# Kernel tuning notes

Measured on AMD Instinct MI355X. Metric: run time of the kernel, lower is better.

The kernel has to match this reference:

```python
import jax, jax.numpy as jnp
import numpy as np

N = 100000   # nodes
E = 1600000  # edges
NEG_SLOPE = 0.2
EPS = 1e-16


def _layer_norm(x, g, b):
    mu = jnp.mean(x, axis=-1, keepdims=True)
    var = jnp.mean((x - mu) ** 2, axis=-1, keepdims=True)
    return (x - mu) * jax.lax.rsqrt(var + 1e-5) * g + b


def _gat_layer(x, W, att_s, att_d, bias, src, dst, heads, C):
    n = x.shape[0]
    h = (x @ W.T).reshape(n, heads, C)            # [N,H,C]
    sa = jnp.sum(h * att_s, axis=-1)              # [N,H]
    da = jnp.sum(h * att_d, axis=-1)              # [N,H]
    logits = jax.nn.leaky_relu(sa[src] + da[dst], NEG_SLOPE)  # [E,H]
    m = jax.ops.segment_max(logits, dst, num_segments=n)      # [N,H]
    m = jnp.where(jnp.isfinite(m), m, 0.0)
    w = jnp.exp(logits - m[dst])                  # [E,H]
    denom = jax.ops.segment_sum(w, dst, num_segments=n)       # [N,H]
    msg = h[src] * w[:, :, None]                  # [E,H,C]
    agg = jax.ops.segment_sum(msg, dst, num_segments=n)       # [N,H,C]
    agg = agg / jnp.maximum(denom, EPS)[:, :, None]
    out = (agg + h).reshape(n, heads * C) + bias  # residual + bias
    return out


def setup_inputs() -> dict:
    key = jax.random.key(0)
    ks = jax.random.split(key, 16)
    s = 0.05
    inp = {
        "x": jax.random.normal(ks[0], (N, 128), jnp.float32),
        "edge_src": jax.random.randint(ks[1], (E,), 0, N, jnp.int32),
        "edge_dst": jax.random.randint(ks[2], (E,), 0, N, jnp.int32),
        # layer 1: in 128 -> heads=2, C=32 (out width 64)
        "W1": jax.random.normal(ks[3], (64, 128), jnp.float32) * s,
        "as1": jax.random.normal(ks[4], (2, 32), jnp.float32) * s,
        "ad1": jax.random.normal(ks[5], (2, 32), jnp.float32) * s,
        "b1": jnp.zeros((64,), jnp.float32),
        # layer 2: 64 -> heads=2, C=32
        "W2": jax.random.normal(ks[6], (64, 64), jnp.float32) * s,
        "as2": jax.random.normal(ks[7], (2, 32), jnp.float32) * s,
        "ad2": jax.random.normal(ks[8], (2, 32), jnp.float32) * s,
        "b2": jnp.zeros((64,), jnp.float32),
        # layer 3 (last): 64 -> heads=1, C=32
        "W3": jax.random.normal(ks[9], (32, 64), jnp.float32) * s,
        "as3": jax.random.normal(ks[10], (1, 32), jnp.float32) * s,
        "ad3": jax.random.normal(ks[11], (1, 32), jnp.float32) * s,
        "b3": jnp.zeros((32,), jnp.float32),
        "gamma1": jnp.ones((64,), jnp.float32),
        "beta1": jnp.zeros((64,), jnp.float32),
        "gamma2": jnp.ones((64,), jnp.float32),
        "beta2": jnp.zeros((64,), jnp.float32),
    }
    return inp


def reference(x, edge_src, edge_dst, W1, as1, ad1, b1, W2, as2, ad2, b2,
              W3, as3, ad3, b3, gamma1, beta1, gamma2, beta2):
    h = _gat_layer(x, W1, as1, ad1, b1, edge_src, edge_dst, 2, 32)
    h = jax.nn.relu(_layer_norm(h, gamma1, beta1))
    h = _gat_layer(h, W2, as2, ad2, b2, edge_src, edge_dst, 2, 32)
    h = jax.nn.relu(_layer_norm(h, gamma2, beta2))
    h = _gat_layer(h, W3, as3, ad3, b3, edge_src, edge_dst, 1, 32)
    return h
```

## Files before the change

kernel.cpp:

```cpp
#include <hip/hip_runtime.h>
#include <hip/hip_fp16.h>

#define LEAKY 0.2f
#define BSH 7
#define BN 128
#define CHUNK 4096
#define NBMAX 1024

__device__ __forceinline__ float leaky(float l) {
  return l >= 0.f ? l : LEAKY * l;
}

typedef _Float16 f16x2 __attribute__((ext_vector_type(2)));

__device__ __forceinline__ float fdot2(unsigned a, unsigned b, float c) {
#if __has_builtin(__builtin_amdgcn_fdot2)
  return __builtin_amdgcn_fdot2(__builtin_bit_cast(f16x2, a),
                                __builtin_bit_cast(f16x2, b), c, false);
#else
  __half2 ha = *(__half2*)&a, hb = *(__half2*)&b;
  float2 fa = __half22float2(ha), fb = __half22float2(hb);
  return fmaf(fa.x, fb.x, fmaf(fa.y, fb.y, c));
#endif
}

__device__ __forceinline__ int packsplat(float w) {
  const __half2 s = __half2half2(__float2half(w));
  return *(const int*)&s;
}
__device__ __forceinline__ __half2 asH2(unsigned u) { return *(__half2*)&u; }

template<int K, int CO, int H, bool IN_F32>
__global__ __launch_bounds__(256, 6)
void gat_gemm3(const void* __restrict__ xin, const float* __restrict__ W,
               const float* __restrict__ atts, const float* __restrict__ attd,
               __half* __restrict__ hh, float* __restrict__ sa, float* __restrict__ da,
               int N) {
  constexpr int CG = CO / 4;
  constexpr int BM = (256 / CG) * 4;
  constexpr int BK = 64;
  constexpr int NK = K / BK;
  constexpr int C = CO / H;
  constexpr int LDW = BK / 2 + 4;

  __shared__ unsigned xs[BM][LDW];
  __shared__ unsigned ws[CO][LDW];

  const int t = (int)threadIdx.x;
  const int cg = t % CG;
  const int ng = t / CG;
  const int n0 = (int)blockIdx.x * BM;

  float acc[4][4] = {};

  for (int kb = 0; kb < NK; ++kb) {
    __syncthreads();
    if constexpr (IN_F32) {
      const float* x = (const float*)xin;
      constexpr int F4R = BK / 4;
      constexpr int TOT = BM * F4R;
      for (int f = t; f < TOT; f += 256) {
        const int r = f / F4R, c = f % F4R;
        int row = n0 + r; row = row < N ? row : N - 1;
        const float4 v = *(const float4*)(x + (size_t)row * K + kb * BK + c * 4);
        const __half2 h0 = __floats2half2_rn(v.x, v.y);
        const __half2 h1 = __floats2half2_rn(v.z, v.w);
        xs[r][c * 2]     = *(const unsigned*)&h0;
        xs[r][c * 2 + 1] = *(const unsigned*)&h1;
      }
    } else {
      const __half* x = (const __half*)xin;
      constexpr int U4R = BK / 8;
      constexpr int TOT = BM * U4R;
      for (int f = t; f < TOT; f += 256) {
        const int r = f / U4R, c = f % U4R;
        int row = n0 + r; row = row < N ? row : N - 1;
        const uint4 v = *(const uint4*)(x + (size_t)row * K + kb * BK + c * 8);
        *(uint4*)&xs[r][c * 4] = v;
      }
    }
    {
      constexpr int F4R = BK / 4;
      constexpr int TOT = CO * F4R;
      for (int f = t; f < TOT; f += 256) {
        const int r = f / F4R, c = f % F4R;
        const float4 v = *(const float4*)(W + (size_t)r * K + kb * BK + c * 4);
        const __half2 h0 = __floats2half2_rn(v.x, v.y);
        const __half2 h1 = __floats2half2_rn(v.z, v.w);
        ws[r][c * 2]     = *(const unsigned*)&h0;
        ws[r][c * 2 + 1] = *(const unsigned*)&h1;
      }
    }
    __syncthreads();
    #pragma unroll
    for (int k = 0; k < BK; k += 8) {
      uint4 xa[4], wb[4];
      #pragma unroll
      for (int i = 0; i < 4; ++i) xa[i] = *(const uint4*)&xs[ng * 4 + i][k / 2];
      #pragma unroll
      for (int j = 0; j < 4; ++j) wb[j] = *(const uint4*)&ws[cg + CG * j][k / 2];
      #pragma unroll
      for (int i = 0; i < 4; ++i) {
        #pragma unroll
        for (int j = 0; j < 4; ++j) {
          acc[i][j] = fdot2(xa[i].x, wb[j].x, acc[i][j]);
          acc[i][j] = fdot2(xa[i].y, wb[j].y, acc[i][j]);
          acc[i][j] = fdot2(xa[i].z, wb[j].z, acc[i][j]);
          acc[i][j] = fdot2(xa[i].w, wb[j].w, acc[i][j]);
        }
      }
    }
  }

  float as_[4], ad_[4];
  #pragma unroll
  for (int j = 0; j < 4; ++j) {
    as_[j] = atts[cg + CG * j];
    ad_[j] = attd[cg + CG * j];
  }
  float ps[4][H] = {}, pd[4][H] = {};
  #pragma unroll
  for (int i = 0; i < 4; ++i) {
    #pragma unroll
    for (int j = 0; j < 4; ++j) {
      const int hd = (CG * j) / C;
      ps[i][hd] = fmaf(acc[i][j], as_[j], ps[i][hd]);
      pd[i][hd] = fmaf(acc[i][j], ad_[j], pd[i][hd]);
    }
  }
  #pragma unroll
  for (int m = 1; m < CG; m <<= 1) {
    #pragma unroll
    for (int i = 0; i < 4; ++i) {
      #pragma unroll
      for (int hd = 0; hd < H; ++hd) {
        ps[i][hd] += __shfl_xor(ps[i][hd], m, 64);
        pd[i][hd] += __shfl_xor(pd[i][hd], m, 64);
      }
    }
  }

  #pragma unroll
  for (int i = 0; i < 4; ++i) {
    const int n = n0 + ng * 4 + i;
    if (n < N) {
      #pragma unroll
      for (int j = 0; j < 4; ++j)
        hh[(size_t)n * CO + cg + CG * j] = __float2half(acc[i][j]);
      if (cg == 0) {
        #pragma unroll
        for (int hd = 0; hd < H; ++hd) {
          sa[n * H + hd] = ps[i][hd];
          da[n * H + hd] = pd[i][hd];
        }
      }
    }
  }
}

__global__ __launch_bounds__(256)
void gat_edge2(const __half* __restrict__ hh,
               const float* __restrict__ sa, const float* __restrict__ da,
               const int* __restrict__ rowp, const int* __restrict__ col,
               const float* __restrict__ bias, const float* __restrict__ gamma,
               const float* __restrict__ beta, __half* __restrict__ out, int N) {
  __shared__ int2 wst[4][4][17][2];
  const int t = (int)threadIdx.x;
  const int lane = t & 63;
  const int wib = t >> 6;
  const int quarter = lane >> 4;
  const int l = lane & 15;
  const int headq = l >> 3;
  const int wgl = (int)((blockIdx.x * blockDim.x + t) >> 6);
  const int n = wgl * 4 + quarter;
  const bool valid = (n < N);
  const int nc = valid ? n : N - 1;
  const int beg = rowp[nc];
  const int end = rowp[nc + 1];
  const float2 dvv = *(const float2*)(da + (size_t)nc * 2);
  const __half2* __restrict__ hhp = (const __half2*)hh;

  const __half2 z = __float2half2_rn(0.f);
  __half2 aL0 = z, aH0 = z, aL1 = z, aH1 = z, aL2 = z, aH2 = z, aL3 = z, aH3 = z;
  __half2 q0 = z, q1 = z;

  int sP = 0; float2 pP = make_float2(0.f, 0.f);
  if (beg < end) {
    const int cnt0 = min(16, end - beg);
    if (l < cnt0) {
      sP = col[beg + l];
      pP = *(const float2*)(sa + (size_t)sP * 2);
    }
  }

  for (int b0 = beg; b0 < end; b0 += 16) {
    const int cnt = min(16, end - b0);
    if (l < cnt) {
      int2 e0; e0.x = sP; e0.y = packsplat(__expf(leaky(pP.x + dvv.x)));
      int2 e1; e1.x = sP; e1.y = packsplat(__expf(leaky(pP.y + dvv.y)));
      wst[wib][quarter][l][0] = e0;
      wst[wib][quarter][l][1] = e1;
    }
    const int nb0 = b0 + 16;
    if (nb0 < end) {
      const int ncnt = min(16, end - nb0);
      if (l < ncnt) {
        sP = col[nb0 + l];
        pP = *(const float2*)(sa + (size_t)sP * 2);
      }
    }
    int i = 0;
    for (; i + 8 <= cnt; i += 8) {
      int2 e[8];
      #pragma unroll
      for (int j = 0; j < 8; ++j) e[j] = wst[wib][quarter][i + j][headq];
      uint2 hv[8];
      #pragma unroll
      for (int j = 0; j < 8; ++j) hv[j] = *(const uint2*)(hhp + ((size_t)e[j].x << 5) + 2 * l);
      __half2 w[8];
      #pragma unroll
      for (int j = 0; j < 8; ++j) w[j] = asH2(e[j].y);
      q0 = __hadd2(q0, __hadd2(__hadd2(w[0], w[1]), __hadd2(w[2], w[3])));
      q1 = __hadd2(q1, __hadd2(__hadd2(w[4], w[5]), __hadd2(w[6], w[7])));
      aL0 = __hfma2(w[0], asH2(hv[0].x), aL0); aH0 = __hfma2(w[0], asH2(hv[0].y), aH0);
      aL1 = __hfma2(w[1], asH2(hv[1].x), aL1); aH1 = __hfma2(w[1], asH2(hv[1].y), aH1);
      aL2 = __hfma2(w[2], asH2(hv[2].x), aL2); aH2 = __hfma2(w[2], asH2(hv[2].y), aH2);
      aL3 = __hfma2(w[3], asH2(hv[3].x), aL3); aH3 = __hfma2(w[3], asH2(hv[3].y), aH3);
      aL0 = __hfma2(w[4], asH2(hv[4].x), aL0); aH0 = __hfma2(w[4], asH2(hv[4].y), aH0);
      aL1 = __hfma2(w[5], asH2(hv[5].x), aL1); aH1 = __hfma2(w[5], asH2(hv[5].y), aH1);
      aL2 = __hfma2(w[6], asH2(hv[6].x), aL2); aH2 = __hfma2(w[6], asH2(hv[6].y), aH2);
      aL3 = __hfma2(w[7], asH2(hv[7].x), aL3); aH3 = __hfma2(w[7], asH2(hv[7].y), aH3);
    }
    for (; i + 4 <= cnt; i += 4) {
      int2 e[4];
      #pragma unroll
      for (int j = 0; j < 4; ++j) e[j] = wst[wib][quarter][i + j][headq];
      uint2 hv[4];
      #pragma unroll
      for (int j = 0; j < 4; ++j) hv[j] = *(const uint2*)(hhp + ((size_t)e[j].x << 5) + 2 * l);
      __half2 w[4];
      #pragma unroll
      for (int j = 0; j < 4; ++j) w[j] = asH2(e[j].y);
      q0 = __hadd2(q0, __hadd2(__hadd2(w[0], w[1]), __hadd2(w[2], w[3])));
      aL0 = __hfma2(w[0], asH2(hv[0].x), aL0); aH0 = __hfma2(w[0], asH2(hv[0].y), aH0);
      aL1 = __hfma2(w[1], asH2(hv[1].x), aL1); aH1 = __hfma2(w[1], asH2(hv[1].y), aH1);
      aL2 = __hfma2(w[2], asH2(hv[2].x), aL2); aH2 = __hfma2(w[2], asH2(hv[2].y), aH2);
      aL3 = __hfma2(w[3], asH2(hv[3].x), aL3); aH3 = __hfma2(w[3], asH2(hv[3].y), aH3);
    }
    for (; i < cnt; ++i) {
      const int2 e = wst[wib][quarter][i][headq];
      const uint2 hv = *(const uint2*)(hhp + ((size_t)e.x << 5) + 2 * l);
      const __half2 w = asH2(e.y);
      q0 = __hadd2(q0, w);
      aL0 = __hfma2(w, asH2(hv.x), aL0);
      aH0 = __hfma2(w, asH2(hv.y), aH0);
    }
  }

  const float c0 = (__low2float(aL0) + __low2float(aL1)) + (__low2float(aL2) + __low2float(aL3));
  const float c1 = (__high2float(aL0) + __high2float(aL1)) + (__high2float(aL2) + __high2float(aL3));
  const float c2 = (__low2float(aH0) + __low2float(aH1)) + (__low2float(aH2) + __low2float(aH3));
  const float c3 = (__high2float(aH0) + __high2float(aH1)) + (__high2float(aH2) + __high2float(aH3));
  const float qf = __low2float(q0) + __low2float(q1);

  const float inv = 1.f / fmaxf(qf, 1e-16f);
  const uint2 hr = *(const uint2*)(hhp + ((size_t)nc << 5) + 2 * l);
  const float2 r01 = __half22float2(asH2(hr.x));
  const float2 r23 = __half22float2(asH2(hr.y));
  const float4 bi = *(const float4*)(bias + 4 * l);
  float v0 = c0 * inv + r01.x + bi.x;
  float v1 = c1 * inv + r01.y + bi.y;
  float v2 = c2 * inv + r23.x + bi.z;
  float v3 = c3 * inv + r23.y + bi.w;
  {
    float s = (v0 + v1) + (v2 + v3);
    #pragma unroll
    for (int m = 1; m < 16; m <<= 1) s += __shfl_xor(s, m, 64);
    const float mu = s * (1.f / 64.f);
    const float d0 = v0 - mu, d1 = v1 - mu, d2 = v2 - mu, d3 = v3 - mu;
    float vs = (d0 * d0 + d1 * d1) + (d2 * d2 + d3 * d3);
    #pragma unroll
    for (int m = 1; m < 16; m <<= 1) vs += __shfl_xor(vs, m, 64);
    const float rs = rsqrtf(vs * (1.f / 64.f) + 1e-5f);
    const float4 g = *(const float4*)(gamma + 4 * l);
    const float4 be = *(const float4*)(beta + 4 * l);
    v0 = fmaxf(d0 * rs * g.x + be.x, 0.f);
    v1 = fmaxf(d1 * rs * g.y + be.y, 0.f);
    v2 = fmaxf(d2 * rs * g.z + be.z, 0.f);
    v3 = fmaxf(d3 * rs * g.w + be.w, 0.f);
  }
  if (valid) {
    const __half2 o01 = __floats2half2_rn(v0, v1);
    const __half2 o23 = __floats2half2_rn(v2, v3);
    uint2 o; o.x = *(const unsigned*)&o01; o.y = *(const unsigned*)&o23;
    *(uint2*)(out + (size_t)n * 64 + 4 * l) = o;
  }
}

__global__ __launch_bounds__(256)
void gat_edge1(const __half* __restrict__ hh,
               const float* __restrict__ sa, const float* __restrict__ da,
               const int* __restrict__ rowp, const int* __restrict__ col,
               const float* __restrict__ bias, float* __restrict__ out, int N) {
  __shared__ int2 wst[4][8][9];
  const int t = (int)threadIdx.x;
  const int lane = t & 63;
  const int wib = t >> 6;
  const int oct = lane >> 3;
  const int l = lane & 7;
  const int wgl = (int)((blockIdx.x * blockDim.x + t) >> 6);
  const int n = wgl * 8 + oct;
  const bool valid = (n < N);
  const int nc = valid ? n : N - 1;
  const int beg = rowp[nc];
  const int end = rowp[nc + 1];
  const float dv = da[nc];
  const __half2* __restrict__ hhp = (const __half2*)hh;

  const __half2 z = __float2half2_rn(0.f);
  __half2 aL0 = z, aH0 = z, aL1 = z, aH1 = z, aL2 = z, aH2 = z, aL3 = z, aH3 = z;
  __half2 q0 = z, q1 = z;

  int sP = 0; float pP = 0.f;
  if (beg < end) {
    const int cnt0 = min(8, end - beg);
    if (l < cnt0) { sP = col[beg + l]; pP = sa[sP]; }
  }

  for (int b0 = beg; b0 < end; b0 += 8) {
    const int cnt = min(8, end - b0);
    if (l < cnt) {
      int2 e; e.x = sP; e.y = packsplat(__expf(leaky(pP + dv)));
      wst[wib][oct][l] = e;
    }
    const int nb0 = b0 + 8;
    if (nb0 < end) {
      const int ncnt = min(8, end - nb0);
      if (l < ncnt) { sP = col[nb0 + l]; pP = sa[sP]; }
    }
    int i = 0;
    for (; i + 8 <= cnt; i += 8) {
      int2 e[8];
      #pragma unroll
      for (int j = 0; j < 8; ++j) e[j] = wst[wib][oct][i + j];
      uint2 hv[8];
      #pragma unroll
      for (int j = 0; j < 8; ++j) hv[j] = *(const uint2*)(hhp + ((size_t)e[j].x << 4) + 2 * l);
      __half2 w[8];
      #pragma unroll
      for (int j = 0; j < 8; ++j) w[j] = asH2(e[j].y);
      q0 = __hadd2(q0, __hadd2(__hadd2(w[0], w[1]), __hadd2(w[2], w[3])));
      q1 = __hadd2(q1, __hadd2(__hadd2(w[4], w[5]), __hadd2(w[6], w[7])));
      aL0 = __hfma2(w[0], asH2(hv[0].x), aL0); aH0 = __hfma2(w[0], asH2(hv[0].y), aH0);
      aL1 = __hfma2(w[1], asH2(hv[1].x), aL1); aH1 = __hfma2(w[1], asH2(hv[1].y), aH1);
      aL2 = __hfma2(w[2], asH2(hv[2].x), aL2); aH2 = __hfma2(w[2], asH2(hv[2].y), aH2);
      aL3 = __hfma2(w[3], asH2(hv[3].x), aL3); aH3 = __hfma2(w[3], asH2(hv[3].y), aH3);
      aL0 = __hfma2(w[4], asH2(hv[4].x), aL0); aH0 = __hfma2(w[4], asH2(hv[4].y), aH0);
      aL1 = __hfma2(w[5], asH2(hv[5].x), aL1); aH1 = __hfma2(w[5], asH2(hv[5].y), aH1);
      aL2 = __hfma2(w[6], asH2(hv[6].x), aL2); aH2 = __hfma2(w[6], asH2(hv[6].y), aH2);
      aL3 = __hfma2(w[7], asH2(hv[7].x), aL3); aH3 = __hfma2(w[7], asH2(hv[7].y), aH3);
    }
    for (; i + 4 <= cnt; i += 4) {
      int2 e[4];
      #pragma unroll
      for (int j = 0; j < 4; ++j) e[j] = wst[wib][oct][i + j];
      uint2 hv[4];
      #pragma unroll
      for (int j = 0; j < 4; ++j) hv[j] = *(const uint2*)(hhp + ((size_t)e[j].x << 4) + 2 * l);
      __half2 w[4];
      #pragma unroll
      for (int j = 0; j < 4; ++j) w[j] = asH2(e[j].y);
      q0 = __hadd2(q0, __hadd2(__hadd2(w[0], w[1]), __hadd2(w[2], w[3])));
      aL0 = __hfma2(w[0], asH2(hv[0].x), aL0); aH0 = __hfma2(w[0], asH2(hv[0].y), aH0);
      aL1 = __hfma2(w[1], asH2(hv[1].x), aL1); aH1 = __hfma2(w[1], asH2(hv[1].y), aH1);
      aL2 = __hfma2(w[2], asH2(hv[2].x), aL2); aH2 = __hfma2(w[2], asH2(hv[2].y), aH2);
      aL3 = __hfma2(w[3], asH2(hv[3].x), aL3); aH3 = __hfma2(w[3], asH2(hv[3].y), aH3);
    }
    for (; i < cnt; ++i) {
      const int2 e = wst[wib][oct][i];
      const uint2 hv = *(const uint2*)(hhp + ((size_t)e.x << 4) + 2 * l);
      const __half2 w = asH2(e.y);
      q0 = __hadd2(q0, w);
      aL0 = __hfma2(w, asH2(hv.x), aL0);
      aH0 = __hfma2(w, asH2(hv.y), aH0);
    }
  }

  const float c0 = (__low2float(aL0) + __low2float(aL1)) + (__low2float(aL2) + __low2float(aL3));
  const float c1 = (__high2float(aL0) + __high2float(aL1)) + (__high2float(aL2) + __high2float(aL3));
  const float c2 = (__low2float(aH0) + __low2float(aH1)) + (__low2float(aH2) + __low2float(aH3));
  const float c3 = (__high2float(aH0) + __high2float(aH1)) + (__high2float(aH2) + __high2float(aH3));
  const float qf = __low2float(q0) + __low2float(q1);

  if (valid) {
    const float inv = 1.f / fmaxf(qf, 1e-16f);
    const uint2 hr = *(const uint2*)(hhp + ((size_t)nc << 4) + 2 * l);
    const float2 r01 = __half22float2(asH2(hr.x));
    const float2 r23 = __half22float2(asH2(hr.y));
    const float4 bi = *(const float4*)(bias + 4 * l);
    float4 o;
    o.x = c0 * inv + r01.x + bi.x;
    o.y = c1 * inv + r01.y + bi.y;
    o.z = c2 * inv + r23.x + bi.z;
    o.w = c3 * inv + r23.y + bi.w;
    *(float4*)(out + (size_t)n * 32 + 4 * l) = o;
  }
}


__global__ __launch_bounds__(256)
void k_hist_chunk(const int* __restrict__ dst, int* __restrict__ cntmat,
                  int E, int NB, int NW) {
  __shared__ int lh[NBMAX];
  const int t = (int)threadIdx.x;
  const int chunk = (int)blockIdx.x;
  const int c0 = chunk * CHUNK;
  const int cnt = min(CHUNK, E - c0);
  for (int b = t; b < NB; b += 256) lh[b] = 0;
  __syncthreads();
  for (int i = t; i < cnt; i += 256)
    atomicAdd(&lh[dst[c0 + i] >> BSH], 1);
  __syncthreads();
  for (int b = t; b < NB; b += 256)
    cntmat[(size_t)b * NW + chunk] = lh[b];
}

template<int VPT>
__global__ __launch_bounds__(256)
void k_colscan(int* __restrict__ cntmat, int* __restrict__ bcnt, int NW) {
  __shared__ int sm[256];
  const int b = (int)blockIdx.x;
  int* row = cntmat + (size_t)b * NW;
  const int t = (int)threadIdx.x;
  int v[VPT];
  int run = 0;
  #pragma unroll
  for (int j = 0; j < VPT; ++j) {
    const int c = t * VPT + j;
    v[j] = (c < NW) ? row[c] : 0;
    run += v[j];
  }
  sm[t] = run;
  __syncthreads();
  #pragma unroll
  for (int off = 1; off < 256; off <<= 1) {
    int xv = (t >= off) ? sm[t - off] : 0;
    __syncthreads();
    sm[t] += xv;
    __syncthreads();
  }
  int excl = sm[t] - run;
  #pragma unroll
  for (int j = 0; j < VPT; ++j) {
    const int c = t * VPT + j;
    if (c < NW) row[c] = excl;
    excl += v[j];
  }
  if (t == 255) bcnt[b] = sm[255];
}

__global__ void k_bscan(const int* __restrict__ bcnt, int nb,
                        int* __restrict__ bstart, int* __restrict__ rowp_last, int E) {
  __shared__ int sm[256];
  const int t = (int)threadIdx.x;
  int v[4];
  #pragma unroll
  for (int j = 0; j < 4; ++j) { int i = t * 4 + j; v[j] = (i < nb) ? bcnt[i] : 0; }
  const int tot = v[0] + v[1] + v[2] + v[3];
  sm[t] = tot; __syncthreads();
  #pragma unroll
  for (int off = 1; off < 256; off <<= 1) {
    int xv = (t >= off) ? sm[t - off] : 0;
    __syncthreads();
    sm[t] += xv;
    __syncthreads();
  }
  int excl = sm[t] - tot;
  #pragma unroll
  for (int j = 0; j < 4; ++j) {
    int i = t * 4 + j;
    if (i < nb) { bstart[i] = excl; excl += v[j]; }
  }
  if (t == 0) { bstart[nb] = E; *rowp_last = E; }
}

__global__ __launch_bounds__(256)
void k_part(const int* __restrict__ src, const int* __restrict__ dst,
            const int* __restrict__ bstart, const int* __restrict__ cntmat,
            int* __restrict__ pairs, int E, int NB, int NW) {
  __shared__ int lh[NBMAX];
  __shared__ int lofs[NBMAX];
  __shared__ int gofs[NBMAX];
  __shared__ int stg[CHUNK];
  __shared__ short stgb[CHUNK];
  __shared__ int bsum[256];
  const int t = (int)threadIdx.x;
  const int chunk = (int)blockIdx.x;
  const int c0 = chunk * CHUNK;
  const int cnt = min(CHUNK, E - c0);

  for (int b = t; b < NB; b += 256) lh[b] = 0;
  __syncthreads();
  for (int i = t; i < cnt; i += 256)
    atomicAdd(&lh[dst[c0 + i] >> BSH], 1);
  __syncthreads();

  int v[4]; int run = 0;
  #pragma unroll
  for (int j = 0; j < 4; ++j) {
    const int b = t * 4 + j;
    v[j] = (b < NB) ? lh[b] : 0;
    run += v[j];
  }
  bsum[t] = run;
  __syncthreads();
  #pragma unroll
  for (int off = 1; off < 256; off <<= 1) {
    int xv = (t >= off) ? bsum[t - off] : 0;
    __syncthreads();
    bsum[t] += xv;
    __syncthreads();
  }
  int base = bsum[t] - run;
  #pragma unroll
  for (int j = 0; j < 4; ++j) {
    const int b = t * 4 + j;
    if (b < NB) lofs[b] = base;
    base += v[j];
  }
  __syncthreads();

  for (int b = t; b < NB; b += 256) {
    gofs[b] = bstart[b] + cntmat[(size_t)b * NW + chunk];
    lh[b] = lofs[b];
  }
  __syncthreads();

  for (int i = t; i < cnt; i += 256) {
    const int d = dst[c0 + i];
    const int b = d >> BSH;
    const int p = atomicAdd(&lh[b], 1);
    stg[p] = (src[c0 + i] << BSH) | (d & (BN - 1));
    stgb[p] = (short)b;
  }
  __syncthreads();

  for (int i = t; i < cnt; i += 256) {
    const int b = (int)stgb[i];
    pairs[gofs[b] + (i - lofs[b])] = stg[i];
  }
}

__global__ __launch_bounds__(256)
void k_bucket_csr(const int* __restrict__ pairs, const int* __restrict__ bstart,
                  int* __restrict__ rowp, int* __restrict__ col, int N) {
  __shared__ int ldeg[BN];
  __shared__ int lofs[BN];
  const int b = (int)blockIdx.x;
  const int t = (int)threadIdx.x;
  const int base = b << BSH;
  const int nn = min(BN, N - base);
  const int s0 = bstart[b];
  const int s1 = bstart[b + 1];

  if (t < BN) ldeg[t] = 0;
  __syncthreads();
  for (int i = s0 + t; i < s1; i += 256)
    atomicAdd(&ldeg[pairs[i] & (BN - 1)], 1);
  __syncthreads();
  if (t < BN) lofs[t] = ldeg[t];
  __syncthreads();
  #pragma unroll
  for (int off = 1; off < BN; off <<= 1) {
    int v = (t < BN && t >= off) ? lofs[t - off] : 0;
    __syncthreads();
    if (t < BN) lofs[t] += v;
    __syncthreads();
  }
  if (t < BN) {
    const int ofs = s0 + lofs[t] - ldeg[t];
    if (t < nn) rowp[base + t] = ofs;
    ldeg[t] = ofs;
  }
  __syncthreads();
  for (int i = s0 + t; i < s1; i += 256) {
    const int pr = pairs[i];
    const int p = atomicAdd(&ldeg[pr & (BN - 1)], 1);
    col[p] = pr >> BSH;
  }
}

extern "C" void kernel_launch(void* const* d_in, const int* in_sizes, int n_in,
                              void* d_out, int out_size, void* d_ws, size_t ws_size,
                              hipStream_t stream) {
  const float* x   = (const float*)d_in[0];
  const int* esrc  = (const int*)d_in[1];
  const int* edst  = (const int*)d_in[2];
  const float* W1  = (const float*)d_in[3];
  const float* as1 = (const float*)d_in[4];
  const float* ad1 = (const float*)d_in[5];
  const float* b1  = (const float*)d_in[6];
  const float* W2  = (const float*)d_in[7];
  const float* as2 = (const float*)d_in[8];
  const float* ad2 = (const float*)d_in[9];
  const float* b2  = (const float*)d_in[10];
  const float* W3  = (const float*)d_in[11];
  const float* as3 = (const float*)d_in[12];
  const float* ad3 = (const float*)d_in[13];
  const float* b3  = (const float*)d_in[14];
  const float* g1  = (const float*)d_in[15];
  const float* be1 = (const float*)d_in[16];
  const float* g2  = (const float*)d_in[17];
  const float* be2 = (const float*)d_in[18];

  const int N = in_sizes[0] / 128;
  const int E = in_sizes[1];
  const int NB = (N + BN - 1) / BN;
  const int NW = (E + CHUNK - 1) / CHUNK;

  char* ws = (char*)d_ws;
  size_t off = 0;
  auto alloc = [&](size_t bytes) -> void* {
    void* p = ws + off;
    off = (off + bytes + 255) & ~(size_t)255;
    return p;
  };
  __half* lnbuf = (__half*)alloc((size_t)N * 64 * 2);
  __half* hh   = (__half*)alloc((size_t)N * 64 * 2);
  float* sab   = (float*)alloc((size_t)N * 2 * 4);
  float* dab   = (float*)alloc((size_t)N * 2 * 4);
  int* rowp    = (int*)alloc((size_t)(N + 1) * 4);
  int* colb    = (int*)alloc((size_t)E * 4);
  int* bcnt    = (int*)alloc((size_t)NB * 4);
  int* bstart  = (int*)alloc((size_t)(NB + 1) * 4);
  int* cntmat  = (int*)alloc((size_t)NB * NW * 4);
  int* pairs = (E <= out_size) ? (int*)d_out : (int*)alloc((size_t)E * 4);
  (void)ws_size; (void)n_in;

  k_hist_chunk<<<NW, 256, 0, stream>>>(edst, cntmat, E, NB, NW);
  if (NW <= 512)        k_colscan<2><<<NB, 256, 0, stream>>>(cntmat, bcnt, NW);
  else if (NW <= 1024)  k_colscan<4><<<NB, 256, 0, stream>>>(cntmat, bcnt, NW);
  else                  k_colscan<8><<<NB, 256, 0, stream>>>(cntmat, bcnt, NW);
  k_bscan<<<1, 256, 0, stream>>>(bcnt, NB, bstart, rowp + N, E);
  k_part<<<NW, 256, 0, stream>>>(esrc, edst, bstart, cntmat, pairs, E, NB, NW);
  k_bucket_csr<<<NB, 256, 0, stream>>>(pairs, bstart, rowp, colb, N);

  const int gG12 = (N + 63) / 64;
  const int gG3  = (N + 127) / 128;
  const int gE2 = (N + 15) / 16;
  const int gE1 = (N + 31) / 32;

  gat_gemm3<128, 64, 2, true><<<gG12, 256, 0, stream>>>(x, W1, as1, ad1, hh, sab, dab, N);
  gat_edge2<<<gE2, 256, 0, stream>>>(hh, sab, dab, rowp, colb, b1, g1, be1, lnbuf, N);

  gat_gemm3<64, 64, 2, false><<<gG12, 256, 0, stream>>>(lnbuf, W2, as2, ad2, hh, sab, dab, N);
  gat_edge2<<<gE2, 256, 0, stream>>>(hh, sab, dab, rowp, colb, b2, g2, be2, lnbuf, N);

  gat_gemm3<64, 32, 1, false><<<gG3, 256, 0, stream>>>(lnbuf, W3, as3, ad3, hh, sab, dab, N);
  gat_edge1<<<gE1, 256, 0, stream>>>(hh, sab, dab, rowp, colb, b3, (float*)d_out, N);
}
```

Baseline: 220.2 us.

## Halve lanes per node in GAT edge kernels using 16-byte feature gathers

The edge aggregation kernels now assign fewer lanes per destination node: 8 lanes per node for the two-head layers (previously 16) and 4 lanes per node for the final layer (previously 8). Each lane gathers 8 halves per neighbour with uint4 loads instead of 4 halves with uint2 loads, and the grids shrink to match. The aim is fewer, wider memory requests per edge and more nodes per wavefront, which should cut per-edge loop overhead and divergence from uneven degrees. In exchange each lane has less unrolling (4 edges per batch instead of 8) and holds more accumulators, and the batch sizes for edge-weight staging shrink.

```diff
diff --git a/kernel.cpp b/kernel.cpp
--- a/kernel.cpp
+++ b/kernel.cpp
@@ -164,249 +164,244 @@
                const int* __restrict__ rowp, const int* __restrict__ col,
                const float* __restrict__ bias, const float* __restrict__ gamma,
                const float* __restrict__ beta, __half* __restrict__ out, int N) {
-  __shared__ int2 wst[4][4][17][2];
-  const int t = (int)threadIdx.x;
-  const int lane = t & 63;
-  const int wib = t >> 6;
-  const int quarter = lane >> 4;
-  const int l = lane & 15;
-  const int headq = l >> 3;
-  const int wgl = (int)((blockIdx.x * blockDim.x + t) >> 6);
-  const int n = wgl * 4 + quarter;
-  const bool valid = (n < N);
-  const int nc = valid ? n : N - 1;
-  const int beg = rowp[nc];
-  const int end = rowp[nc + 1];
-  const float2 dvv = *(const float2*)(da + (size_t)nc * 2);
-  const __half2* __restrict__ hhp = (const __half2*)hh;
-
-  const __half2 z = __float2half2_rn(0.f);
-  __half2 aL0 = z, aH0 = z, aL1 = z, aH1 = z, aL2 = z, aH2 = z, aL3 = z, aH3 = z;
-  __half2 q0 = z, q1 = z;
-
-  int sP = 0; float2 pP = make_float2(0.f, 0.f);
-  if (beg < end) {
-    const int cnt0 = min(16, end - beg);
-    if (l < cnt0) {
-      sP = col[beg + l];
-      pP = *(const float2*)(sa + (size_t)sP * 2);
-    }
-  }
-
-  for (int b0 = beg; b0 < end; b0 += 16) {
-    const int cnt = min(16, end - b0);
-    if (l < cnt) {
-      int2 e0; e0.x = sP; e0.y = packsplat(__expf(leaky(pP.x + dvv.x)));
-      int2 e1; e1.x = sP; e1.y = packsplat(__expf(leaky(pP.y + dvv.y)));
-      wst[wib][quarter][l][0] = e0;
-      wst[wib][quarter][l][1] = e1;
-    }
-    const int nb0 = b0 + 16;
-    if (nb0 < end) {
-      const int ncnt = min(16, end - nb0);
-      if (l < ncnt) {
-        sP = col[nb0 + l];
-        pP = *(const float2*)(sa + (size_t)sP * 2);
-      }
-    }
-    int i = 0;
-    for (; i + 8 <= cnt; i += 8) {
-      int2 e[8];
-      #pragma unroll
-      for (int j = 0; j < 8; ++j) e[j] = wst[wib][quarter][i + j][headq];
-      uint2 hv[8];
-      #pragma unroll
-      for (int j = 0; j < 8; ++j) hv[j] = *(const uint2*)(hhp + ((size_t)e[j].x << 5) + 2 * l);
-      __half2 w[8];
-      #pragma unroll
-      for (int j = 0; j < 8; ++j) w[j] = asH2(e[j].y);
-      q0 = __hadd2(q0, __hadd2(__hadd2(w[0], w[1]), __hadd2(w[2], w[3])));
-      q1 = __hadd2(q1, __hadd2(__hadd2(w[4], w[5]), __hadd2(w[6], w[7])));
-      aL0 = __hfma2(w[0], asH2(hv[0].x), aL0); aH0 = __hfma2(w[0], asH2(hv[0].y), aH0);
-      aL1 = __hfma2(w[1], asH2(hv[1].x), aL1); aH1 = __hfma2(w[1], asH2(hv[1].y), aH1);
-      aL2 = __hfma2(w[2], asH2(hv[2].x), aL2); aH2 = __hfma2(w[2], asH2(hv[2].y), aH2);
-      aL3 = __hfma2(w[3], asH2(hv[3].x), aL3); aH3 = __hfma2(w[3], asH2(hv[3].y), aH3);
-      aL0 = __hfma2(w[4], asH2(hv[4].x), aL0); aH0 = __hfma2(w[4], asH2(hv[4].y), aH0);
-      aL1 = __hfma2(w[5], asH2(hv[5].x), aL1); aH1 = __hfma2(w[5], asH2(hv[5].y), aH1);
-      aL2 = __hfma2(w[6], asH2(hv[6].x), aL2); aH2 = __hfma2(w[6], asH2(hv[6].y), aH2);
-      aL3 = __hfma2(w[7], asH2(hv[7].x), aL3); aH3 = __hfma2(w[7], asH2(hv[7].y), aH3);
-    }
-    for (; i + 4 <= cnt; i += 4) {
-      int2 e[4];
-      #pragma unroll
-      for (int j = 0; j < 4; ++j) e[j] = wst[wib][quarter][i + j][headq];
-      uint2 hv[4];
-      #pragma unroll
-      for (int j = 0; j < 4; ++j) hv[j] = *(const uint2*)(hhp + ((size_t)e[j].x << 5) + 2 * l);
-      __half2 w[4];
-      #pragma unroll
-      for (int j = 0; j < 4; ++j) w[j] = asH2(e[j].y);
-      q0 = __hadd2(q0, __hadd2(__hadd2(w[0], w[1]), __hadd2(w[2], w[3])));
-      aL0 = __hfma2(w[0], asH2(hv[0].x), aL0); aH0 = __hfma2(w[0], asH2(hv[0].y), aH0);
-      aL1 = __hfma2(w[1], asH2(hv[1].x), aL1); aH1 = __hfma2(w[1], asH2(hv[1].y), aH1);
-      aL2 = __hfma2(w[2], asH2(hv[2].x), aL2); aH2 = __hfma2(w[2], asH2(hv[2].y), aH2);
-      aL3 = __hfma2(w[3], asH2(hv[3].x), aL3); aH3 = __hfma2(w[3], asH2(hv[3].y), aH3);
-    }
-    for (; i < cnt; ++i) {
-      const int2 e = wst[wib][quarter][i][headq];
-      const uint2 hv = *(const uint2*)(hhp + ((size_t)e.x << 5) + 2 * l);
-      const __half2 w = asH2(e.y);
-      q0 = __hadd2(q0, w);
-      aL0 = __hfma2(w, asH2(hv.x), aL0);
-      aH0 = __hfma2(w, asH2(hv.y), aH0);
-    }
-  }
-
-  const float c0 = (__low2float(aL0) + __low2float(aL1)) + (__low2float(aL2) + __low2float(aL3));
-  const float c1 = (__high2float(aL0) + __high2float(aL1)) + (__high2float(aL2) + __high2float(aL3));
-  const float c2 = (__low2float(aH0) + __low2float(aH1)) + (__low2float(aH2) + __low2float(aH3));
-  const float c3 = (__high2float(aH0) + __high2float(aH1)) + (__high2float(aH2) + __high2float(aH3));
-  const float qf = __low2float(q0) + __low2float(q1);
-
-  const float inv = 1.f / fmaxf(qf, 1e-16f);
-  const uint2 hr = *(const uint2*)(hhp + ((size_t)nc << 5) + 2 * l);
-  const float2 r01 = __half22float2(asH2(hr.x));
-  const float2 r23 = __half22float2(asH2(hr.y));
-  const float4 bi = *(const float4*)(bias + 4 * l);
-  float v0 = c0 * inv + r01.x + bi.x;
-  float v1 = c1 * inv + r01.y + bi.y;
-  float v2 = c2 * inv + r23.x + bi.z;
-  float v3 = c3 * inv + r23.y + bi.w;
-  {
-    float s = (v0 + v1) + (v2 + v3);
-    #pragma unroll
-    for (int m = 1; m < 16; m <<= 1) s += __shfl_xor(s, m, 64);
-    const float mu = s * (1.f / 64.f);
-    const float d0 = v0 - mu, d1 = v1 - mu, d2 = v2 - mu, d3 = v3 - mu;
-    float vs = (d0 * d0 + d1 * d1) + (d2 * d2 + d3 * d3);
-    #pragma unroll
-    for (int m = 1; m < 16; m <<= 1) vs += __shfl_xor(vs, m, 64);
-    const float rs = rsqrtf(vs * (1.f / 64.f) + 1e-5f);
-    const float4 g = *(const float4*)(gamma + 4 * l);
-    const float4 be = *(const float4*)(beta + 4 * l);
-    v0 = fmaxf(d0 * rs * g.x + be.x, 0.f);
-    v1 = fmaxf(d1 * rs * g.y + be.y, 0.f);
-    v2 = fmaxf(d2 * rs * g.z + be.z, 0.f);
-    v3 = fmaxf(d3 * rs * g.w + be.w, 0.f);
-  }
-  if (valid) {
-    const __half2 o01 = __floats2half2_rn(v0, v1);
-    const __half2 o23 = __floats2half2_rn(v2, v3);
-    uint2 o; o.x = *(const unsigned*)&o01; o.y = *(const unsigned*)&o23;
-    *(uint2*)(out + (size_t)n * 64 + 4 * l) = o;
-  }
-}
-
-__global__ __launch_bounds__(256)
-void gat_edge1(const __half* __restrict__ hh,
-               const float* __restrict__ sa, const float* __restrict__ da,
-               const int* __restrict__ rowp, const int* __restrict__ col,
-               const float* __restrict__ bias, float* __restrict__ out, int N) {
-  __shared__ int2 wst[4][8][9];
+  __shared__ int2 wst[4][8][9][2];
   const int t = (int)threadIdx.x;
   const int lane = t & 63;
   const int wib = t >> 6;
   const int oct = lane >> 3;
   const int l = lane & 7;
+  const int headq = l >> 2;
   const int wgl = (int)((blockIdx.x * blockDim.x + t) >> 6);
   const int n = wgl * 8 + oct;
   const bool valid = (n < N);
   const int nc = valid ? n : N - 1;
   const int beg = rowp[nc];
   const int end = rowp[nc + 1];
-  const float dv = da[nc];
-  const __half2* __restrict__ hhp = (const __half2*)hh;
+  const float2 dvv = *(const float2*)(da + (size_t)nc * 2);
+  const __half* __restrict__ hp = hh;
 
   const __half2 z = __float2half2_rn(0.f);
-  __half2 aL0 = z, aH0 = z, aL1 = z, aH1 = z, aL2 = z, aH2 = z, aL3 = z, aH3 = z;
-  __half2 q0 = z, q1 = z;
-
-  int sP = 0; float pP = 0.f;
+  __half2 A0 = z, A1 = z, A2 = z, A3 = z;
+  __half2 B0 = z, B1 = z, B2 = z, B3 = z;
+  __half2 qA = z, qB = z;
+
+  int sP = 0; float2 pP = make_float2(0.f, 0.f);
   if (beg < end) {
-    const int cnt0 = min(8, end - beg);
-    if (l < cnt0) { sP = col[beg + l]; pP = sa[sP]; }
+    const int c0 = min(8, end - beg);
+    if (l < c0) { sP = col[beg + l]; pP = *(const float2*)(sa + (size_t)sP * 2); }
   }
 
   for (int b0 = beg; b0 < end; b0 += 8) {
     const int cnt = min(8, end - b0);
     if (l < cnt) {
-      int2 e; e.x = sP; e.y = packsplat(__expf(leaky(pP + dv)));
-      wst[wib][oct][l] = e;
+      int2 e0; e0.x = sP; e0.y = packsplat(__expf(leaky(pP.x + dvv.x)));
+      int2 e1; e1.x = sP; e1.y = packsplat(__expf(leaky(pP.y + dvv.y)));
+      wst[wib][oct][l][0] = e0;
+      wst[wib][oct][l][1] = e1;
     }
     const int nb0 = b0 + 8;
     if (nb0 < end) {
       const int ncnt = min(8, end - nb0);
+      if (l < ncnt) { sP = col[nb0 + l]; pP = *(const float2*)(sa + (size_t)sP * 2); }
+    }
+    int i = 0;
+    for (; i + 4 <= cnt; i += 4) {
+      const int2 e0 = wst[wib][oct][i][headq];
+      const int2 e1 = wst[wib][oct][i + 1][headq];
+      const int2 e2 = wst[wib][oct][i + 2][headq];
+      const int2 e3 = wst[wib][oct][i + 3][headq];
+      const uint4 h0 = *(const uint4*)(hp + ((size_t)e0.x << 6) + 8 * l);
+      const uint4 h1 = *(const uint4*)(hp + ((size_t)e1.x << 6) + 8 * l);
+      const uint4 h2 = *(const uint4*)(hp + ((size_t)e2.x << 6) + 8 * l);
+      const uint4 h3 = *(const uint4*)(hp + ((size_t)e3.x << 6) + 8 * l);
+      const __half2 w0 = asH2(e0.y), w1 = asH2(e1.y), w2 = asH2(e2.y), w3 = asH2(e3.y);
+      qA = __hadd2(qA, __hadd2(w0, w1));
+      qB = __hadd2(qB, __hadd2(w2, w3));
+      A0 = __hfma2(w0, asH2(h0.x), A0); A1 = __hfma2(w0, asH2(h0.y), A1);
+      A2 = __hfma2(w0, asH2(h0.z), A2); A3 = __hfma2(w0, asH2(h0.w), A3);
+      B0 = __hfma2(w1, asH2(h1.x), B0); B1 = __hfma2(w1, asH2(h1.y), B1);
+      B2 = __hfma2(w1, asH2(h1.z), B2); B3 = __hfma2(w1, asH2(h1.w), B3);
+      A0 = __hfma2(w2, asH2(h2.x), A0); A1 = __hfma2(w2, asH2(h2.y), A1);
+      A2 = __hfma2(w2, asH2(h2.z), A2); A3 = __hfma2(w2, asH2(h2.w), A3);
+      B0 = __hfma2(w3, asH2(h3.x), B0); B1 = __hfma2(w3, asH2(h3.y), B1);
+      B2 = __hfma2(w3, asH2(h3.z), B2); B3 = __hfma2(w3, asH2(h3.w), B3);
+    }
+    for (; i < cnt; ++i) {
+      const int2 e = wst[wib][oct][i][headq];
+      const uint4 hv = *(const uint4*)(hp + ((size_t)e.x << 6) + 8 * l);
+      const __half2 w = asH2(e.y);
+      qA = __hadd2(qA, w);
+      A0 = __hfma2(w, asH2(hv.x), A0); A1 = __hfma2(w, asH2(hv.y), A1);
+      A2 = __hfma2(w, asH2(hv.z), A2); A3 = __hfma2(w, asH2(hv.w), A3);
+    }
+  }
+
+  const float c0 = __low2float(A0) + __low2float(B0);
+  const float c1 = __high2float(A0) + __high2float(B0);
+  const float c2 = __low2float(A1) + __low2float(B1);
+  const float c3 = __high2float(A1) + __high2float(B1);
+  const float c4 = __low2float(A2) + __low2float(B2);
+  const float c5 = __high2float(A2) + __high2float(B2);
+  const float c6 = __low2float(A3) + __low2float(B3);
+  const float c7 = __high2float(A3) + __high2float(B3);
+  const float qf = __low2float(qA) + __low2float(qB);
+
+  const float inv = 1.f / fmaxf(qf, 1e-16f);
+  const uint4 hr = *(const uint4*)(hp + ((size_t)nc << 6) + 8 * l);
+  const float2 r0 = __half22float2(asH2(hr.x));
+  const float2 r1 = __half22float2(asH2(hr.y));
+  const float2 r2 = __half22float2(asH2(hr.z));
+  const float2 r3 = __half22float2(asH2(hr.w));
+  const float4 bi0 = *(const float4*)(bias + 8 * l);
+  const float4 bi1 = *(const float4*)(bias + 8 * l + 4);
+  float v0 = c0 * inv + r0.x + bi0.x;
+  float v1 = c1 * inv + r0.y + bi0.y;
+  float v2 = c2 * inv + r1.x + bi0.z;
+  float v3 = c3 * inv + r1.y + bi0.w;
+  float v4 = c4 * inv + r2.x + bi1.x;
+  float v5 = c5 * inv + r2.y + bi1.y;
+  float v6 = c6 * inv + r3.x + bi1.z;
+  float v7 = c7 * inv + r3.y + bi1.w;
+  {
+    float s = ((v0 + v1) + (v2 + v3)) + ((v4 + v5) + (v6 + v7));
+    s += __shfl_xor(s, 1, 64); s += __shfl_xor(s, 2, 64); s += __shfl_xor(s, 4, 64);
+    const float mu = s * (1.f / 64.f);
+    const float d0 = v0 - mu, d1 = v1 - mu, d2 = v2 - mu, d3 = v3 - mu;
+    const float d4 = v4 - mu, d5 = v5 - mu, d6 = v6 - mu, d7 = v7 - mu;
+    float vs = ((d0 * d0 + d1 * d1) + (d2 * d2 + d3 * d3)) +
+               ((d4 * d4 + d5 * d5) + (d6 * d6 + d7 * d7));
+    vs += __shfl_xor(vs, 1, 64); vs += __shfl_xor(vs, 2, 64); vs += __shfl_xor(vs, 4, 64);
+    const float rs = rsqrtf(vs * (1.f / 64.f) + 1e-5f);
+    const float4 g0 = *(const float4*)(gamma + 8 * l);
+    const float4 g1 = *(const float4*)(gamma + 8 * l + 4);
+    const float4 e0 = *(const float4*)(beta + 8 * l);
+    const float4 e1 = *(const float4*)(beta + 8 * l + 4);
+    v0 = fmaxf(d0 * rs * g0.x + e0.x, 0.f);
+    v1 = fmaxf(d1 * rs * g0.y + e0.y, 0.f);
+    v2 = fmaxf(d2 * rs * g0.z + e0.z, 0.f);
+    v3 = fmaxf(d3 * rs * g0.w + e0.w, 0.f);
+    v4 = fmaxf(d4 * rs * g1.x + e1.x, 0.f);
+    v5 = fmaxf(d5 * rs * g1.y + e1.y, 0.f);
+    v6 = fmaxf(d6 * rs * g1.z + e1.z, 0.f);
+    v7 = fmaxf(d7 * rs * g1.w + e1.w, 0.f);
+  }
+  if (valid) {
+    const __half2 o0 = __floats2half2_rn(v0, v1);
+    const __half2 o1 = __floats2half2_rn(v2, v3);
+    const __half2 o2 = __floats2half2_rn(v4, v5);
+    const __half2 o3 = __floats2half2_rn(v6, v7);
+    uint4 o;
+    o.x = *(const unsigned*)&o0; o.y = *(const unsigned*)&o1;
+    o.z = *(const unsigned*)&o2; o.w = *(const unsigned*)&o3;
+    *(uint4*)(out + (size_t)n * 64 + 8 * l) = o;
+  }
+}
+
+__global__ __launch_bounds__(256)
+void gat_edge1(const __half* __restrict__ hh,
+               const float* __restrict__ sa, const float* __restrict__ da,
+               const int* __restrict__ rowp, const int* __restrict__ col,
+               const float* __restrict__ bias, float* __restrict__ out, int N) {
+  __shared__ int2 wst[4][16][5];
+  const int t = (int)threadIdx.x;
+  const int lane = t & 63;
+  const int wib = t >> 6;
+  const int nq = lane >> 2;
+  const int l = lane & 3;
+  const int wgl = (int)((blockIdx.x * blockDim.x + t) >> 6);
+  const int n = wgl * 16 + nq;
+  const bool valid = (n < N);
+  const int nc = valid ? n : N - 1;
+  const int beg = rowp[nc];
+  const int end = rowp[nc + 1];
+  const float dv = da[nc];
+  const __half* __restrict__ hp = hh;
+
+  const __half2 z = __float2half2_rn(0.f);
+  __half2 A0 = z, A1 = z, A2 = z, A3 = z;
+  __half2 B0 = z, B1 = z, B2 = z, B3 = z;
+  __half2 qA = z, qB = z;
+
+  int sP = 0; float pP = 0.f;
+  if (beg < end) {
+    const int c0 = min(4, end - beg);
+    if (l < c0) { sP = col[beg + l]; pP = sa[sP]; }
+  }
+
+  for (int b0 = beg; b0 < end; b0 += 4) {
+    const int cnt = min(4, end - b0);
+    if (l < cnt) {
+      int2 e; e.x = sP; e.y = packsplat(__expf(leaky(pP + dv)));
+      wst[wib][nq][l] = e;
+    }
+    const int nb0 = b0 + 4;
+    if (nb0 < end) {
+      const int ncnt = min(4, end - nb0);
       if (l < ncnt) { sP = col[nb0 + l]; pP = sa[sP]; }
     }
-    int i = 0;
-    for (; i + 8 <= cnt; i += 8) {
-      int2 e[8];
-      #pragma unroll
-      for (int j = 0; j < 8; ++j) e[j] = wst[wib][oct][i + j];
-      uint2 hv[8];
-      #pragma unroll
-      for (int j = 0; j < 8; ++j) hv[j] = *(const uint2*)(hhp + ((size_t)e[j].x << 4) + 2 * l);
-      __half2 w[8];
-      #pragma unroll
-      for (int j = 0; j < 8; ++j) w[j] = asH2(e[j].y);
-      q0 = __hadd2(q0, __hadd2(__hadd2(w[0], w[1]), __hadd2(w[2], w[3])));
-      q1 = __hadd2(q1, __hadd2(__hadd2(w[4], w[5]), __hadd2(w[6], w[7])));
-      aL0 = __hfma2(w[0], asH2(hv[0].x), aL0); aH0 = __hfma2(w[0], asH2(hv[0].y), aH0);
-      aL1 = __hfma2(w[1], asH2(hv[1].x), aL1); aH1 = __hfma2(w[1], asH2(hv[1].y), aH1);
-      aL2 = __hfma2(w[2], asH2(hv[2].x), aL2); aH2 = __hfma2(w[2], asH2(hv[2].y), aH2);
-      aL3 = __hfma2(w[3], asH2(hv[3].x), aL3); aH3 = __hfma2(w[3], asH2(hv[3].y), aH3);
-      aL0 = __hfma2(w[4], asH2(hv[4].x), aL0); aH0 = __hfma2(w[4], asH2(hv[4].y), aH0);
-      aL1 = __hfma2(w[5], asH2(hv[5].x), aL1); aH1 = __hfma2(w[5], asH2(hv[5].y), aH1);
-      aL2 = __hfma2(w[6], asH2(hv[6].x), aL2); aH2 = __hfma2(w[6], asH2(hv[6].y), aH2);
-      aL3 = __hfma2(w[7], asH2(hv[7].x), aL3); aH3 = __hfma2(w[7], asH2(hv[7].y), aH3);
-    }
-    for (; i + 4 <= cnt; i += 4) {
-      int2 e[4];
-      #pragma unroll
-      for (int j = 0; j < 4; ++j) e[j] = wst[wib][oct][i + j];
-      uint2 hv[4];
-      #pragma unroll
-      for (int j = 0; j < 4; ++j) hv[j] = *(const uint2*)(hhp + ((size_t)e[j].x << 4) + 2 * l);
-      __half2 w[4];
-      #pragma unroll
-      for (int j = 0; j < 4; ++j) w[j] = asH2(e[j].y);
-      q0 = __hadd2(q0, __hadd2(__hadd2(w[0], w[1]), __hadd2(w[2], w[3])));
-      aL0 = __hfma2(w[0], asH2(hv[0].x), aL0); aH0 = __hfma2(w[0], asH2(hv[0].y), aH0);
-      aL1 = __hfma2(w[1], asH2(hv[1].x), aL1); aH1 = __hfma2(w[1], asH2(hv[1].y), aH1);
-      aL2 = __hfma2(w[2], asH2(hv[2].x), aL2); aH2 = __hfma2(w[2], asH2(hv[2].y), aH2);
-      aL3 = __hfma2(w[3], asH2(hv[3].x), aL3); aH3 = __hfma2(w[3], asH2(hv[3].y), aH3);
-    }
-    for (; i < cnt; ++i) {
-      const int2 e = wst[wib][oct][i];
-      const uint2 hv = *(const uint2*)(hhp + ((size_t)e.x << 4) + 2 * l);
-      const __half2 w = asH2(e.y);
-      q0 = __hadd2(q0, w);
-      aL0 = __hfma2(w, asH2(hv.x), aL0);
-      aH0 = __hfma2(w, asH2(hv.y), aH0);
-    }
-  }
-
-  const float c0 = (__low2float(aL0) + __low2float(aL1)) + (__low2float(aL2) + __low2float(aL3));
-  const float c1 = (__high2float(aL0) + __high2float(aL1)) + (__high2float(aL2) + __high2float(aL3));
-  const float c2 = (__low2float(aH0) + __low2float(aH1)) + (__low2float(aH2) + __low2float(aH3));
-  const float c3 = (__high2float(aH0) + __high2float(aH1)) + (__high2float(aH2) + __high2float(aH3));
-  const float qf = __low2float(q0) + __low2float(q1);
+    if (cnt == 4) {
+      const int2 e0 = wst[wib][nq][0];
+      const int2 e1 = wst[wib][nq][1];
+      const int2 e2 = wst[wib][nq][2];
+      const int2 e3 = wst[wib][nq][3];
+      const uint4 h0 = *(const uint4*)(hp + ((size_t)e0.x << 5) + 8 * l);
+      const uint4 h1 = *(const uint4*)(hp + ((size_t)e1.x << 5) + 8 * l);
+      const uint4 h2 = *(const uint4*)(hp + ((size_t)e2.x << 5) + 8 * l);
+      const uint4 h3 = *(const uint4*)(hp + ((size_t)e3.x << 5) + 8 * l);
+      const __half2 w0 = asH2(e0.y), w1 = asH2(e1.y), w2 = asH2(e2.y), w3 = asH2(e3.y);
+      qA = __hadd2(qA, __hadd2(w0, w1));
+      qB = __hadd2(qB, __hadd2(w2, w3));
+      A0 = __hfma2(w0, asH2(h0.x), A0); A1 = __hfma2(w0, asH2(h0.y), A1);
+      A2 = __hfma2(w0, asH2(h0.z), A2); A3 = __hfma2(w0, asH2(h0.w), A3);
+      B0 = __hfma2(w1, asH2(h1.x), B0); B1 = __hfma2(w1, asH2(h1.y), B1);
+      B2 = __hfma2(w1, asH2(h1.z), B2); B3 = __hfma2(w1, asH2(h1.w), B3);
+      A0 = __hfma2(w2, asH2(h2.x), A0); A1 = __hfma2(w2, asH2(h2.y), A1);
+      A2 = __hfma2(w2, asH2(h2.z), A2); A3 = __hfma2(w2, asH2(h2.w), A3);
+      B0 = __hfma2(w3, asH2(h3.x), B0); B1 = __hfma2(w3, asH2(h3.y), B1);
+      B2 = __hfma2(w3, asH2(h3.z), B2); B3 = __hfma2(w3, asH2(h3.w), B3);
+    } else {
+      for (int i = 0; i < cnt; ++i) {
+        const int2 e = wst[wib][nq][i];
+        const uint4 hv = *(const uint4*)(hp + ((size_t)e.x << 5) + 8 * l);
+        const __half2 w = asH2(e.y);
+        qA = __hadd2(qA, w);
+        A0 = __hfma2(w, asH2(hv.x), A0); A1 = __hfma2(w, asH2(hv.y), A1);
+        A2 = __hfma2(w, asH2(hv.z), A2); A3 = __hfma2(w, asH2(hv.w), A3);
+      }
+    }
+  }
 
   if (valid) {
+    const float c0 = __low2float(A0) + __low2float(B0);
+    const float c1 = __high2float(A0) + __high2float(B0);
+    const float c2 = __low2float(A1) + __low2float(B1);
+    const float c3 = __high2float(A1) + __high2float(B1);
+    const float c4 = __low2float(A2) + __low2float(B2);
+    const float c5 = __high2float(A2) + __high2float(B2);
+    const float c6 = __low2float(A3) + __low2float(B3);
+    const float c7 = __high2float(A3) + __high2float(B3);
+    const float qf = __low2float(qA) + __low2float(qB);
     const float inv = 1.f / fmaxf(qf, 1e-16f);
-    const uint2 hr = *(const uint2*)(hhp + ((size_t)nc << 4) + 2 * l);
-    const float2 r01 = __half22float2(asH2(hr.x));
-    const float2 r23 = __half22float2(asH2(hr.y));
-    const float4 bi = *(const float4*)(bias + 4 * l);
-    float4 o;
-    o.x = c0 * inv + r01.x + bi.x;
-    o.y = c1 * inv + r01.y + bi.y;
-    o.z = c2 * inv + r23.x + bi.z;
-    o.w = c3 * inv + r23.y + bi.w;
-    *(float4*)(out + (size_t)n * 32 + 4 * l) = o;
-  }
-}
-
+    const uint4 hr = *(const uint4*)(hp + ((size_t)nc << 5) + 8 * l);
+    const float2 r0 = __half22float2(asH2(hr.x));
+    const float2 r1 = __half22float2(asH2(hr.y));
+    const float2 r2 = __half22float2(asH2(hr.z));
+    const float2 r3 = __half22float2(asH2(hr.w));
+    const float4 bi0 = *(const float4*)(bias + 8 * l);
+    const float4 bi1 = *(const float4*)(bias + 8 * l + 4);
+    float4 oA, oB;
+    oA.x = c0 * inv + r0.x + bi0.x;
+    oA.y = c1 * inv + r0.y + bi0.y;
+    oA.z = c2 * inv + r1.x + bi0.z;
+    oA.w = c3 * inv + r1.y + bi0.w;
+    oB.x = c4 * inv + r2.x + bi1.x;
+    oB.y = c5 * inv + r2.y + bi1.y;
+    oB.z = c6 * inv + r3.x + bi1.z;
+    oB.w = c7 * inv + r3.y + bi1.w;
+    *(float4*)(out + (size_t)n * 32 + 8 * l) = oA;
+    *(float4*)(out + (size_t)n * 32 + 8 * l + 4) = oB;
+  }
+}
 
 __global__ __launch_bounds__(256)
 void k_hist_chunk(const int* __restrict__ dst, int* __restrict__ cntmat,
@@ -647,8 +642,8 @@
 
   const int gG12 = (N + 63) / 64;
   const int gG3  = (N + 127) / 128;
-  const int gE2 = (N + 15) / 16;
-  const int gE1 = (N + 31) / 32;
+  const int gE2 = (N + 31) / 32;
+  const int gE1 = (N + 63) / 64;
 
   gat_gemm3<128, 64, 2, true><<<gG12, 256, 0, stream>>>(x, W1, as1, ad1, hh, sab, dab, N);
   gat_edge2<<<gE2, 256, 0, stream>>>(hh, sab, dab, rowp, colb, b1, g1, be1, lnbuf, N);
```

Measured after the change: 216.1 us. No clear change (-1.9%).
